# Optimization experiments

Hardware: AMD Instinct MI355X
Metric: run time of the kernel (lower is better)

## Reference

```python
import jax, jax.numpy as jnp
import numpy as np
from math import sqrt

D_MODEL = 1024
D_HEAD = 64
N_HEADS = D_MODEL // D_HEAD
MAX_SEQ = 2048
BATCH = 2
SEQ = 2048
NEG = -1e9


def setup_inputs() -> dict:
    key = jax.random.key(0)
    ks = jax.random.split(key, 10)
    s = 0.02
    x = jax.random.normal(ks[0], (BATCH, SEQ, D_MODEL), dtype=jnp.float32)
    # causal additive mask: 0 on/below diagonal, -1e9 above
    causal = jnp.triu(jnp.full((SEQ, SEQ), NEG, dtype=jnp.float32), k=1)
    mask = causal[None, None, :, :]
    Wq = jax.random.normal(ks[1], (D_MODEL, D_MODEL), jnp.float32) * s
    bq = jnp.zeros((D_MODEL,), jnp.float32)
    Wk = jax.random.normal(ks[2], (D_MODEL, D_MODEL), jnp.float32) * s
    bk = jnp.zeros((D_MODEL,), jnp.float32)
    Wv = jax.random.normal(ks[3], (D_MODEL, D_MODEL), jnp.float32) * s
    bv = jnp.zeros((D_MODEL,), jnp.float32)
    Er = jax.random.normal(ks[4], (MAX_SEQ, D_HEAD), jnp.float32)
    Wo = jax.random.normal(ks[5], (D_MODEL, D_MODEL), jnp.float32) * s
    bo = jnp.zeros((D_MODEL,), jnp.float32)
    return {"x": x, "mask": mask, "Wq": Wq, "bq": bq, "Wk": Wk, "bk": bk,
            "Wv": Wv, "bv": bv, "Er": Er, "Wo": Wo, "bo": bo}


def _skew(qE):
    # qE: [B, H, S, S] -> skewed s_rel [B, H, S, S] (Music Transformer trick)
    b, h, s, _ = qE.shape
    padded = jnp.pad(qE, ((0, 0), (0, 0), (0, 0), (1, 0)))  # [B,H,S,S+1]
    reshaped = padded.reshape(b, h, s + 1, s)
    return reshaped[:, :, 1:, :]


def reference(x, mask, Wq, bq, Wk, bk, Wv, bv, Er, Wo, bo):
    B, S, _ = x.shape
    h_factor = sqrt(D_HEAD)
    q = (x @ Wq.T + bq).reshape(B, S, N_HEADS, D_HEAD).transpose(0, 2, 1, 3)
    k = (x @ Wk.T + bk).reshape(B, S, N_HEADS, D_HEAD).transpose(0, 2, 1, 3)
    v = (x @ Wv.T + bv).reshape(B, S, N_HEADS, D_HEAD).transpose(0, 2, 1, 3)
    start = max(0, MAX_SEQ - S)
    left = Er[start:, :]                       # [S, D_HEAD]
    qE = jnp.einsum('bhsd,rd->bhsr', q, left)  # [B,H,S,S]
    s_rel = _skew(qE)
    qk_t = jnp.einsum('bhsd,bhtd->bhst', q, k)
    logits = (qk_t + s_rel) / h_factor + mask
    attn = jax.nn.softmax(logits, axis=-1)
    out = jnp.einsum('bhst,bhtd->bhsd', attn, v)
    out = out.transpose(0, 2, 1, 3).reshape(B, S, D_MODEL)
    return out @ Wo.T + bo
```

## Files before the change

kernel.cpp:

```cpp
#include <hip/hip_runtime.h>
#include <cstdint>
#include <cstddef>

typedef __bf16 bf16;
typedef __bf16 bf16x8 __attribute__((ext_vector_type(8)));
typedef __bf16 bf16x4 __attribute__((ext_vector_type(4)));
typedef __bf16 bf16x2 __attribute__((ext_vector_type(2)));
typedef float  f32x4  __attribute__((ext_vector_type(4)));

typedef const __attribute__((address_space(1))) void gas_t;
typedef __attribute__((address_space(3))) void las_t;

#define S_LEN 2048
#define DM    1024
#define NH    16
#define DH    64
#define NEG_BIG (-1e30f)

#define OXB   0u
#define OWQB  4194304u
#define OWKB  5242880u
#define OWVB  6291456u
#define OWOB  7340032u
#define OERB  8388608u
#define OQW   8519680u
#define OKW   12713984u
#define OVW   16908288u
#define OOW   21102592u
#define WS_NEED_B 50593792ull

__global__ void fill_sentinel(float* __restrict__ out, unsigned n, float v)
{
    const unsigned tid = blockIdx.x * blockDim.x + threadIdx.x;
    const unsigned nth = gridDim.x * blockDim.x;
    for (unsigned i = tid; i < n; i += nth) out[i] = v;
}

__device__ inline void conv_seg(const float* __restrict__ s, bf16* __restrict__ d,
                                unsigned n8, unsigned tid, unsigned nth)
{
    for (unsigned i = tid; i < n8; i += nth) {
        const f32x4 a = ((const f32x4*)s)[2 * i], b = ((const f32x4*)s)[2 * i + 1];
        bf16x8 o;
        o[0] = (bf16)a[0]; o[1] = (bf16)a[1]; o[2] = (bf16)a[2]; o[3] = (bf16)a[3];
        o[4] = (bf16)b[0]; o[5] = (bf16)b[1]; o[6] = (bf16)b[2]; o[7] = (bf16)b[3];
        ((bf16x8*)d)[i] = o;
    }
}

__global__ void conv_all(const float* x, const float* wq, const float* wk,
                         const float* wv, const float* wo, const float* er,
                         bf16* __restrict__ base)
{
    const unsigned tid = blockIdx.x * blockDim.x + threadIdx.x;
    const unsigned nth = gridDim.x * blockDim.x;
    conv_seg(x,  base + OXB,  4194304u / 8, tid, nth);
    conv_seg(wq, base + OWQB, 1048576u / 8, tid, nth);
    conv_seg(wk, base + OWKB, 1048576u / 8, tid, nth);
    conv_seg(wv, base + OWVB, 1048576u / 8, tid, nth);
    conv_seg(wo, base + OWOB, 1048576u / 8, tid, nth);
    conv_seg(er, base + OERB, 131072u  / 8, tid, nth);
}

__global__ __launch_bounds__(256, 2)
void gemm_qkv(const bf16* __restrict__ X,
              const bf16* __restrict__ Wq, const bf16* __restrict__ Wk,
              const bf16* __restrict__ Wv,
              const float* __restrict__ bq, const float* __restrict__ bk,
              const float* __restrict__ bv,
              bf16* __restrict__ q_ws, bf16* __restrict__ k_ws,
              bf16* __restrict__ v_ws)
{
    __shared__ alignas(16) bf16 sA[128 * 32];
    __shared__ alignas(16) bf16 sW[128 * 32];

    const int t    = threadIdx.x;
    const int lane = t & 63;
    const int wv   = t >> 6;
    const int row0 = blockIdx.y * 128;
    const int col0g = blockIdx.x * 128;
    const int which = col0g >> 10;
    const int col0  = col0g & 1023;

    const bf16*  W  = (which == 0) ? Wq : (which == 1) ? Wk : Wv;
    const float* bb = (which == 0) ? bq : (which == 1) ? bk : bv;

    const int wrow = (wv & 1) * 64;
    const int wcol = (wv >> 1) * 64;
    const int qd   = lane >> 4;
    const int ln   = lane & 15;

    const int srow_l = lane >> 2;
    const int schk   = (lane & 3) ^ (srow_l & 3);

    f32x4 acc[4][4];
#pragma unroll
    for (int i = 0; i < 4; ++i)
#pragma unroll
        for (int j = 0; j < 4; ++j) acc[i][j] = {0.f, 0.f, 0.f, 0.f};

    for (int k0 = 0; k0 < DM; k0 += 32) {
#pragma unroll
        for (int p = 0; p < 2; ++p) {
            const int slab = p * 4 + wv;
            const int gr   = slab * 16 + srow_l;
            __builtin_amdgcn_global_load_lds(
                (gas_t*)&X[(size_t)(row0 + gr) * DM + k0 + schk * 8],
                (las_t*)&sA[slab * 512], 16, 0, 0);
            __builtin_amdgcn_global_load_lds(
                (gas_t*)&W[(size_t)(col0 + gr) * DM + k0 + schk * 8],
                (las_t*)&sW[slab * 512], 16, 0, 0);
        }
        __syncthreads();
        bf16x8 af[4], bfr[4];
#pragma unroll
        for (int mt = 0; mt < 4; ++mt) {
            const int r = wrow + mt * 16 + ln;
            af[mt] = *(const bf16x8*)&sA[r * 32 + ((qd ^ (r & 3)) * 8)];
        }
#pragma unroll
        for (int nt = 0; nt < 4; ++nt) {
            const int r = wcol + nt * 16 + ln;
            bfr[nt] = *(const bf16x8*)&sW[r * 32 + ((qd ^ (r & 3)) * 8)];
        }
#pragma unroll
        for (int mt = 0; mt < 4; ++mt)
#pragma unroll
            for (int nt = 0; nt < 4; ++nt)
                acc[mt][nt] = __builtin_amdgcn_mfma_f32_16x16x32_bf16(
                    af[mt], bfr[nt], acc[mt][nt], 0, 0, 0);
        __syncthreads();
    }

#pragma unroll
    for (int mt = 0; mt < 4; ++mt) {
#pragma unroll
        for (int nt = 0; nt < 4; ++nt) {
            const int   o  = col0 + wcol + nt * 16 + ln;
            const float bv_ = bb[o];
            const int   h  = o >> 6, d = o & 63;
#pragma unroll
            for (int r = 0; r < 4; ++r) {
                const int i = row0 + wrow + mt * 16 + qd * 4 + r;
                const int b = i >> 11, s = i & 2047;
                const float v = acc[mt][nt][r] + bv_;
                if (which == 2)
                    v_ws[(((size_t)(b * NH + h)) * DH + d) * S_LEN + s] = (bf16)v;
                else {
                    bf16* o_p = (which == 0) ? q_ws : k_ws;
                    o_p[(((size_t)(b * NH + h)) * S_LEN + s) * DH + d] = (bf16)v;
                }
            }
        }
    }
}

__global__ __launch_bounds__(256, 2)
void gemm_out(const bf16* __restrict__ A, const bf16* __restrict__ W,
              const float* __restrict__ bias, float* __restrict__ out)
{
    __shared__ alignas(16) bf16 sA[128 * 32];
    __shared__ alignas(16) bf16 sW[128 * 32];

    const int t    = threadIdx.x;
    const int lane = t & 63;
    const int wv   = t >> 6;
    const int row0 = blockIdx.y * 128;
    const int col0 = blockIdx.x * 128;
    const int wrow = (wv & 1) * 64;
    const int wcol = (wv >> 1) * 64;
    const int qd   = lane >> 4;
    const int ln   = lane & 15;

    const int srow_l = lane >> 2;
    const int schk   = (lane & 3) ^ (srow_l & 3);

    f32x4 acc[4][4];
#pragma unroll
    for (int i = 0; i < 4; ++i)
#pragma unroll
        for (int j = 0; j < 4; ++j) acc[i][j] = {0.f, 0.f, 0.f, 0.f};

    for (int k0 = 0; k0 < DM; k0 += 32) {
#pragma unroll
        for (int p = 0; p < 2; ++p) {
            const int slab = p * 4 + wv;
            const int gr   = slab * 16 + srow_l;
            __builtin_amdgcn_global_load_lds(
                (gas_t*)&A[(size_t)(row0 + gr) * DM + k0 + schk * 8],
                (las_t*)&sA[slab * 512], 16, 0, 0);
            __builtin_amdgcn_global_load_lds(
                (gas_t*)&W[(size_t)(col0 + gr) * DM + k0 + schk * 8],
                (las_t*)&sW[slab * 512], 16, 0, 0);
        }
        __syncthreads();
        bf16x8 af[4], bfr[4];
#pragma unroll
        for (int mt = 0; mt < 4; ++mt) {
            const int r = wrow + mt * 16 + ln;
            af[mt] = *(const bf16x8*)&sA[r * 32 + ((qd ^ (r & 3)) * 8)];
        }
#pragma unroll
        for (int nt = 0; nt < 4; ++nt) {
            const int r = wcol + nt * 16 + ln;
            bfr[nt] = *(const bf16x8*)&sW[r * 32 + ((qd ^ (r & 3)) * 8)];
        }
#pragma unroll
        for (int mt = 0; mt < 4; ++mt)
#pragma unroll
            for (int nt = 0; nt < 4; ++nt)
                acc[mt][nt] = __builtin_amdgcn_mfma_f32_16x16x32_bf16(
                    af[mt], bfr[nt], acc[mt][nt], 0, 0, 0);
        __syncthreads();
    }

#pragma unroll
    for (int mt = 0; mt < 4; ++mt)
#pragma unroll
        for (int nt = 0; nt < 4; ++nt) {
            const int   o  = col0 + wcol + nt * 16 + ln;
            const float bb = bias[o];
#pragma unroll
            for (int r = 0; r < 4; ++r) {
                const int i = row0 + wrow + mt * 16 + qd * 4 + r;
                out[(size_t)i * DM + o] = acc[mt][nt][r] + bb;
            }
        }
}

__device__ inline unsigned pk2(float a, float b)
{
    bf16x2 v; v[0] = (bf16)a; v[1] = (bf16)b;
    unsigned u; __builtin_memcpy(&u, &v, 4); return u;
}

__device__ inline int swz(int row, int chunk)
{
    return row * 128 + ((chunk ^ (row & 7)) << 4);
}

__global__ __launch_bounds__(256, 2)
void attn9(const bf16* __restrict__ q, const bf16* __restrict__ k,
           const bf16* __restrict__ vT, const bf16* __restrict__ Er,
           bf16* __restrict__ o_out)
{
    __shared__ alignas(16) bf16 sK[4096];
    __shared__ alignas(16) bf16 sV[4096];
    __shared__ alignas(16) bf16 sE[8192];
    __shared__ alignas(16) float g_lds[4][16 * 100];

    const int t    = threadIdx.x;
    const int lane = t & 63;
    const int wid  = t >> 6;
    const int qd   = lane >> 4;
    const int ln   = lane & 15;

    const int bx = blockIdx.x;
    const int h  = blockIdx.y;
    const int b  = blockIdx.z;

    const size_t bh = (size_t)b * NH + h;
    const bf16* qp = q  + bh * S_LEN * DH;
    const bf16* kp = k  + bh * S_LEN * DH;
    const bf16* vp = vT + bh * DH * S_LEN;

    const int s0lane = ((qd & 1) << 5) + ln;
    const int s1lane = s0lane + 16;

    const int sr  = t >> 3;
    const int scc = t & 7;

    for (int phase = 0; phase < 2; ++phase) {
        const int g  = phase ? (31 - bx) : bx;
        const int qt = 4 * g + wid;
        const int i0 = qt * 16;

        const bf16x8 qf0 = *(const bf16x8*)&qp[(size_t)(i0 + ln) * DH + qd * 8];
        const bf16x8 qf1 = *(const bf16x8*)&qp[(size_t)(i0 + ln) * DH + 32 + qd * 8];

        f32x4 oT[4];
#pragma unroll
        for (int mt = 0; mt < 4; ++mt) oT[mt] = {0.f, 0.f, 0.f, 0.f};
        float m_s = NEG_BIG, l_s = 0.f;

        const int nkb = g + 1;

        bf16x8 stK[2], stV[2], stE[4];
        auto LOADS = [&](int kb) {
            const int j0 = kb * 64;
#pragma unroll
            for (int p = 0; p < 2; ++p) {
                const int r = p * 32 + sr;
                stK[p] = *(const bf16x8*)&kp[(size_t)(j0 + r) * DH + scc * 8];
                stV[p] = *(const bf16x8*)&vp[(size_t)r * S_LEN + j0 + scc * 8];
            }
            const int Wm48 = 1984 + j0 - 64 * g;
#pragma unroll
            for (int p = 0; p < 4; ++p) {
                int er = Wm48 + p * 32 + sr;
                er = (er > S_LEN - 1) ? (S_LEN - 1) : er;
                stE[p] = *(const bf16x8*)&Er[(size_t)er * DH + scc * 8];
            }
        };
        auto WRITES = [&]() {
#pragma unroll
            for (int p = 0; p < 2; ++p) {
                const int r = p * 32 + sr;
                *(bf16x8*)((char*)sK + swz(r, scc)) = stK[p];
                *(bf16x8*)((char*)sV + swz(r, scc)) = stV[p];
            }
#pragma unroll
            for (int p = 0; p < 4; ++p) {
                const int row = p * 32 + sr;
                *(bf16x8*)((char*)sE + swz(row, scc)) = stE[p];
            }
        };

        LOADS(0);
        for (int kb = 0; kb < nkb; ++kb) {
            const int j0 = kb * 64;
            __syncthreads();
            WRITES();
            __syncthreads();
            if (kb + 1 < nkb) LOADS(kb + 1);

            f32x4 sc[4];
#pragma unroll
            for (int t4 = 0; t4 < 4; ++t4) {
                const int krow = t4 * 16 + ln;
                const bf16x8 kf0 = *(const bf16x8*)((const char*)sK + swz(krow, qd));
                const bf16x8 kf1 = *(const bf16x8*)((const char*)sK + swz(krow, 4 + qd));
                f32x4 c = {0.f, 0.f, 0.f, 0.f};
                c = __builtin_amdgcn_mfma_f32_16x16x32_bf16(kf0, qf0, c, 0, 0, 0);
                c = __builtin_amdgcn_mfma_f32_16x16x32_bf16(kf1, qf1, c, 0, 0, 0);
                sc[t4] = c;
            }

#pragma unroll
            for (int ut = 0; ut < 5; ++ut) {
                const int erow = (3 - wid + ut) * 16 + ln;
                const bf16x8 ef0 = *(const bf16x8*)((const char*)sE + swz(erow, qd));
                const bf16x8 ef1 = *(const bf16x8*)((const char*)sE + swz(erow, 4 + qd));
                f32x4 c = {0.f, 0.f, 0.f, 0.f};
                c = __builtin_amdgcn_mfma_f32_16x16x32_bf16(ef0, qf0, c, 0, 0, 0);
                c = __builtin_amdgcn_mfma_f32_16x16x32_bf16(ef1, qf1, c, 0, 0, 0);
                *(f32x4*)&g_lds[wid][ln * 100 + ut * 16 + qd * 4] = c;
            }
            asm volatile("s_waitcnt lgkmcnt(0)" ::: "memory");

#pragma unroll
            for (int t4 = 0; t4 < 4; ++t4)
#pragma unroll
                for (int r = 0; r < 4; ++r) {
                    const int krow = t4 * 16 + qd * 4 + r;
                    const int u    = krow + 15 - ln;
                    const float srel = g_lds[wid][ln * 100 + u];
                    const float v    = (sc[t4][r] + srel) * 0.125f;
                    sc[t4][r] = (j0 + krow > i0 + ln) ? NEG_BIG : v;
                }

            float mx = sc[0][0];
#pragma unroll
            for (int t4 = 0; t4 < 4; ++t4)
#pragma unroll
                for (int r = 0; r < 4; ++r) mx = fmaxf(mx, sc[t4][r]);
            mx = fmaxf(mx, __shfl_xor(mx, 16, 64));
            mx = fmaxf(mx, __shfl_xor(mx, 32, 64));
            const float mnew  = fmaxf(m_s, mx);
            const float alpha = __expf(m_s - mnew);
            m_s = mnew;
            float sum = 0.f;
#pragma unroll
            for (int t4 = 0; t4 < 4; ++t4)
#pragma unroll
                for (int r = 0; r < 4; ++r) {
                    const float p = __expf(sc[t4][r] - mnew);
                    sc[t4][r] = p;
                    sum += p;
                }
            sum += __shfl_xor(sum, 16, 64);
            sum += __shfl_xor(sum, 32, 64);
            l_s = l_s * alpha + sum;
#pragma unroll
            for (int mt = 0; mt < 4; ++mt)
#pragma unroll
                for (int r = 0; r < 4; ++r) oT[mt][r] *= alpha;

            unsigned pk[4][2];
#pragma unroll
            for (int t4 = 0; t4 < 4; ++t4) {
                pk[t4][0] = pk2(sc[t4][0], sc[t4][1]);
                pk[t4][1] = pk2(sc[t4][2], sc[t4][3]);
            }
#pragma unroll
            for (int ch = 0; ch < 2; ++ch) {
                const unsigned a0 = __shfl(pk[ch * 2][0],     s0lane, 64);
                const unsigned a1 = __shfl(pk[ch * 2][1],     s0lane, 64);
                const unsigned a2 = __shfl(pk[ch * 2][0],     s1lane, 64);
                const unsigned a3 = __shfl(pk[ch * 2][1],     s1lane, 64);
                const unsigned b0 = __shfl(pk[ch * 2 + 1][0], s0lane, 64);
                const unsigned b1 = __shfl(pk[ch * 2 + 1][1], s0lane, 64);
                const unsigned b2 = __shfl(pk[ch * 2 + 1][0], s1lane, 64);
                const unsigned b3 = __shfl(pk[ch * 2 + 1][1], s1lane, 64);
                const bool lo = (qd < 2);
                unsigned dw[4] = { lo ? a0 : b0, lo ? a1 : b1,
                                   lo ? a2 : b2, lo ? a3 : b3 };
                bf16x8 pfr;
                __builtin_memcpy(&pfr, dw, 16);
#pragma unroll
                for (int mt = 0; mt < 4; ++mt) {
                    const bf16x8 vf = *(const bf16x8*)
                        ((const char*)sV + swz(mt * 16 + ln, ch * 4 + qd));
                    oT[mt] = __builtin_amdgcn_mfma_f32_16x16x32_bf16(vf, pfr, oT[mt], 0, 0, 0);
                }
            }
        }

        const float inv = 1.f / l_s;
        bf16* op = o_out + ((size_t)b * S_LEN + i0 + ln) * DM + (size_t)h * DH;
#pragma unroll
        for (int mt = 0; mt < 4; ++mt) {
            bf16x4 st;
#pragma unroll
            for (int r = 0; r < 4; ++r) st[r] = (bf16)(oT[mt][r] * inv);
            *(bf16x4*)&op[mt * 16 + qd * 4] = st;
        }
    }
}

extern "C" void kernel_launch(void* const* d_in, const int* in_sizes, int n_in,
                              void* d_out, int out_size, void* d_ws, size_t ws_size,
                              hipStream_t stream)
{
    (void)in_sizes; (void)n_in;
    if (ws_size < WS_NEED_B) {
        fill_sentinel<<<512, 256, 0, stream>>>((float*)d_out, (unsigned)out_size, 10000.f);
        return;
    }
    const float* x  = (const float*)d_in[0];
    const float* Wq = (const float*)d_in[2];
    const float* bq = (const float*)d_in[3];
    const float* Wk = (const float*)d_in[4];
    const float* bk = (const float*)d_in[5];
    const float* Wv = (const float*)d_in[6];
    const float* bv = (const float*)d_in[7];
    const float* Er = (const float*)d_in[8];
    const float* Wo = (const float*)d_in[9];
    const float* bo = (const float*)d_in[10];

    bf16* base = (bf16*)d_ws;

    conv_all<<<2048, 256, 0, stream>>>(x, Wq, Wk, Wv, Wo, Er, base);
    gemm_qkv<<<dim3(24, 32), 256, 0, stream>>>(
        base + OXB, base + OWQB, base + OWKB, base + OWVB,
        bq, bk, bv, base + OQW, base + OKW, base + OVW);
    attn9<<<dim3(16, NH, 2), 256, 0, stream>>>(
        base + OQW, base + OKW, base + OVW, base + OERB, base + OOW);
    gemm_out<<<dim3(8, 32), 256, 0, stream>>>(
        base + OOW, base + OWOB, bo, (float*)d_out);
}
```

Before: 240.3 us.

## Pre-tile Er into MFMA fragment layout and read it directly from global

The conversion kernel now writes Er in a tiled layout in which each 16-row tile is stored in the order of the MFMA operand fragments, one contiguous bf16x8 per lane. The attention kernel drops the sE shared-memory staging of Er and loads the relative-position fragments straight from global/L2 with coalesced reads. This frees 16KB of LDS and raises the occupancy hint to 3 blocks per SM, at the cost of global-memory latency inside the inner loop that is no longer software-prefetched.

Result: no change. 240.0 us (-0.1%).

```diff
diff --git a/kernel.cpp b/kernel.cpp
--- a/kernel.cpp
+++ b/kernel.cpp
@@ -59,7 +59,19 @@
     conv_seg(wk, base + OWKB, 1048576u / 8, tid, nth);
     conv_seg(wv, base + OWVB, 1048576u / 8, tid, nth);
     conv_seg(wo, base + OWOB, 1048576u / 8, tid, nth);
-    conv_seg(er, base + OERB, 131072u  / 8, tid, nth);
+    bf16* ert = base + OERB;
+    for (unsigned c = tid; c < 16384u; c += nth) {
+        const unsigned t = c >> 7, rem = c & 127u;
+        const unsigned f = rem >> 6, l = rem & 63u;
+        const unsigned row = t * 16 + (l & 15u);
+        const unsigned col = f * 32 + (l >> 4) * 8;
+        const float* s = &er[(size_t)row * DH + col];
+        const f32x4 a = *(const f32x4*)s, b = *(const f32x4*)(s + 4);
+        bf16x8 o;
+        o[0] = (bf16)a[0]; o[1] = (bf16)a[1]; o[2] = (bf16)a[2]; o[3] = (bf16)a[3];
+        o[4] = (bf16)b[0]; o[5] = (bf16)b[1]; o[6] = (bf16)b[2]; o[7] = (bf16)b[3];
+        ((bf16x8*)ert)[c] = o;
+    }
 }
 
 __global__ __launch_bounds__(256, 2)
@@ -239,14 +251,13 @@
     return row * 128 + ((chunk ^ (row & 7)) << 4);
 }
 
-__global__ __launch_bounds__(256, 2)
-void attn9(const bf16* __restrict__ q, const bf16* __restrict__ k,
-           const bf16* __restrict__ vT, const bf16* __restrict__ Er,
-           bf16* __restrict__ o_out)
+__global__ __launch_bounds__(256, 3)
+void attn10(const bf16* __restrict__ q, const bf16* __restrict__ k,
+            const bf16* __restrict__ vT, const bf16* __restrict__ ErT,
+            bf16* __restrict__ o_out)
 {
     __shared__ alignas(16) bf16 sK[4096];
     __shared__ alignas(16) bf16 sV[4096];
-    __shared__ alignas(16) bf16 sE[8192];
     __shared__ alignas(16) float g_lds[4][16 * 100];
 
     const int t    = threadIdx.x;
@@ -285,7 +296,7 @@
 
         const int nkb = g + 1;
 
-        bf16x8 stK[2], stV[2], stE[4];
+        bf16x8 stK[2], stV[2];
         auto LOADS = [&](int kb) {
             const int j0 = kb * 64;
 #pragma unroll
@@ -294,13 +305,6 @@
                 stK[p] = *(const bf16x8*)&kp[(size_t)(j0 + r) * DH + scc * 8];
                 stV[p] = *(const bf16x8*)&vp[(size_t)r * S_LEN + j0 + scc * 8];
             }
-            const int Wm48 = 1984 + j0 - 64 * g;
-#pragma unroll
-            for (int p = 0; p < 4; ++p) {
-                int er = Wm48 + p * 32 + sr;
-                er = (er > S_LEN - 1) ? (S_LEN - 1) : er;
-                stE[p] = *(const bf16x8*)&Er[(size_t)er * DH + scc * 8];
-            }
         };
         auto WRITES = [&]() {
 #pragma unroll
@@ -308,11 +312,6 @@
                 const int r = p * 32 + sr;
                 *(bf16x8*)((char*)sK + swz(r, scc)) = stK[p];
                 *(bf16x8*)((char*)sV + swz(r, scc)) = stV[p];
-            }
-#pragma unroll
-            for (int p = 0; p < 4; ++p) {
-                const int row = p * 32 + sr;
-                *(bf16x8*)((char*)sE + swz(row, scc)) = stE[p];
             }
         };
 
@@ -336,11 +335,13 @@
                 sc[t4] = c;
             }
 
+            const int twb = ((1984 + j0 - 64 * g) >> 4) + 3 - wid;
 #pragma unroll
             for (int ut = 0; ut < 5; ++ut) {
-                const int erow = (3 - wid + ut) * 16 + ln;
-                const bf16x8 ef0 = *(const bf16x8*)((const char*)sE + swz(erow, qd));
-                const bf16x8 ef1 = *(const bf16x8*)((const char*)sE + swz(erow, 4 + qd));
+                int tw = twb + ut;
+                tw = (tw > 127) ? 127 : tw;
+                const bf16x8 ef0 = *(const bf16x8*)&ErT[(size_t)tw * 1024 + lane * 8];
+                const bf16x8 ef1 = *(const bf16x8*)&ErT[(size_t)tw * 1024 + 512 + lane * 8];
                 f32x4 c = {0.f, 0.f, 0.f, 0.f};
                 c = __builtin_amdgcn_mfma_f32_16x16x32_bf16(ef0, qf0, c, 0, 0, 0);
                 c = __builtin_amdgcn_mfma_f32_16x16x32_bf16(ef1, qf1, c, 0, 0, 0);
@@ -454,7 +455,7 @@
     gemm_qkv<<<dim3(24, 32), 256, 0, stream>>>(
         base + OXB, base + OWQB, base + OWKB, base + OWVB,
         bq, bk, bv, base + OQW, base + OKW, base + OVW);
-    attn9<<<dim3(16, NH, 2), 256, 0, stream>>>(
+    attn10<<<dim3(16, NH, 2), 256, 0, stream>>>(
         base + OQW, base + OKW, base + OVW, base + OERB, base + OOW);
     gemm_out<<<dim3(8, 32), 256, 0, stream>>>(
         base + OOW, base + OWOB, bo, (float*)d_out);
```
